# Performance work log

Hardware: AMD Instinct MI355X
Metric: run time of the kernel (lower is better)

The kernel has to match this reference:

```python
import jax, jax.numpy as jnp
import numpy as np

N_NODES = 4096
N_EDGES = 131072
IN_DIM = 40
HID = 128
OUT = 128
GAT_H = 2
GAT_C = 64
D_MODEL = 128
N_HEAD = 4
FF_DIM = 2048
N_LAYERS = 2
EPS = 1e-5
NEG_SLOPE = 0.2


def _layer_norm(x, g, b):
    mu = x.mean(-1, keepdims=True)
    var = ((x - mu) ** 2).mean(-1, keepdims=True)
    return (x - mu) / jnp.sqrt(var + EPS) * g + b


def _gat_conv(h, src, dst, W, a_src, a_dst, bias):
    # PyG GATConv, concat=True, eval mode (no dropout). Self loops already in (src, dst).
    N = h.shape[0]
    xw = (h @ W.T).reshape(N, GAT_H, GAT_C)          # [N, H, C]
    al_src = (xw * a_src).sum(-1)                     # [N, H]
    al_dst = (xw * a_dst).sum(-1)                     # [N, H]
    e = jax.nn.leaky_relu(al_src[src] + al_dst[dst], NEG_SLOPE)  # [E, H]
    # segment softmax over incoming edges of each dst node
    m = jax.ops.segment_max(e, dst, num_segments=N)
    ex = jnp.exp(e - m[dst])
    s = jax.ops.segment_sum(ex, dst, num_segments=N)
    alpha = ex / (s[dst] + 1e-16)                     # [E, H]
    out = jax.ops.segment_sum(xw[src] * alpha[..., None], dst, num_segments=N)
    return out.reshape(N, GAT_H * GAT_C) + bias


def _encoder_layer(x, p):
    # post-norm nn.TransformerEncoderLayer, relu FFN, eval mode
    (in_w, in_b, out_w, out_b, ln1_g, ln1_b,
     ff_w1, ff_b1, ff_w2, ff_b2, ln2_g, ln2_b) = p
    S, E = x.shape
    Dh = E // N_HEAD
    qkv = x @ in_w.T + in_b                           # [S, 3E]
    q, k, v = [t.reshape(S, N_HEAD, Dh) for t in jnp.split(qkv, 3, axis=-1)]
    scores = jnp.einsum('shd,thd->hst', q, k) / jnp.asarray(np.sqrt(Dh), x.dtype)
    attn = jax.nn.softmax(scores, axis=-1)            # [H, S, S]
    o = jnp.einsum('hst,thd->shd', attn, v).reshape(S, E) @ out_w.T + out_b
    x = _layer_norm(x + o, ln1_g, ln1_b)
    ff = jax.nn.relu(x @ ff_w1.T + ff_b1) @ ff_w2.T + ff_b2
    return _layer_norm(x + ff, ln2_g, ln2_b)


def _forward(floats, edge_index):
    (x, enc_w1, enc_b1, enc_w2, enc_b2,
     gat_w, gat_asrc, gat_adst, gat_b,
     l0_in_w, l0_in_b, l0_out_w, l0_out_b, l0_ln1_g, l0_ln1_b,
     l0_ff_w1, l0_ff_b1, l0_ff_w2, l0_ff_b2, l0_ln2_g, l0_ln2_b,
     l1_in_w, l1_in_b, l1_out_w, l1_out_b, l1_ln1_g, l1_ln1_b,
     l1_ff_w1, l1_ff_b1, l1_ff_w2, l1_ff_b2, l1_ln2_g, l1_ln2_b) = floats
    N = x.shape[0]
    # encoder MLP
    h = jax.nn.relu(x @ enc_w1.T + enc_b1) @ enc_w2.T + enc_b2
    # add one self loop per node (GATConv add_self_loops semantics)
    loop = jnp.arange(N, dtype=edge_index.dtype)
    src = jnp.concatenate([edge_index[0], loop])
    dst = jnp.concatenate([edge_index[1], loop])
    h = _gat_conv(h, src, dst, gat_w, gat_asrc, gat_adst, gat_b)
    layers = [
        (l0_in_w, l0_in_b, l0_out_w, l0_out_b, l0_ln1_g, l0_ln1_b,
         l0_ff_w1, l0_ff_b1, l0_ff_w2, l0_ff_b2, l0_ln2_g, l0_ln2_b),
        (l1_in_w, l1_in_b, l1_out_w, l1_out_b, l1_ln1_g, l1_ln1_b,
         l1_ff_w1, l1_ff_b1, l1_ff_w2, l1_ff_b2, l1_ln2_g, l1_ln2_b),
    ]
    for p in layers:
        h = _encoder_layer(h, p)
    return h


def setup_inputs() -> dict:
    key = jax.random.key(0)
    ks = jax.random.split(key, 40)
    s = 0.05
    inp = {}
    inp['x'] = jax.random.normal(ks[0], (N_NODES, IN_DIM), dtype=jnp.float32)
    # edges with src != dst (self loops added inside reference)
    src = jax.random.randint(ks[1], (N_EDGES,), 0, N_NODES)
    off = jax.random.randint(ks[2], (N_EDGES,), 1, N_NODES)
    dst = (src + off) % N_NODES
    inp['edge_index'] = jnp.stack([src, dst]).astype(jnp.int64)
    inp['enc_w1'] = jax.random.normal(ks[3], (HID, IN_DIM)) * s
    inp['enc_b1'] = jnp.zeros((HID,), jnp.float32)
    inp['enc_w2'] = jax.random.normal(ks[4], (OUT, HID)) * s
    inp['enc_b2'] = jnp.zeros((OUT,), jnp.float32)
    inp['gat_w'] = jax.random.normal(ks[5], (GAT_H * GAT_C, OUT)) * s
    inp['gat_asrc'] = jax.random.normal(ks[6], (GAT_H, GAT_C)) * s
    inp['gat_adst'] = jax.random.normal(ks[7], (GAT_H, GAT_C)) * s
    inp['gat_b'] = jnp.zeros((GAT_H * GAT_C,), jnp.float32)
    for i in range(N_LAYERS):
        k = jax.random.split(ks[8 + i], 8)
        inp[f'l{i}_in_w'] = jax.random.normal(k[0], (3 * D_MODEL, D_MODEL)) * s
        inp[f'l{i}_in_b'] = jnp.zeros((3 * D_MODEL,), jnp.float32)
        inp[f'l{i}_out_w'] = jax.random.normal(k[1], (D_MODEL, D_MODEL)) * s
        inp[f'l{i}_out_b'] = jnp.zeros((D_MODEL,), jnp.float32)
        inp[f'l{i}_ln1_g'] = jnp.ones((D_MODEL,), jnp.float32)
        inp[f'l{i}_ln1_b'] = jnp.zeros((D_MODEL,), jnp.float32)
        inp[f'l{i}_ff_w1'] = jax.random.normal(k[2], (FF_DIM, D_MODEL)) * s
        inp[f'l{i}_ff_b1'] = jnp.zeros((FF_DIM,), jnp.float32)
        inp[f'l{i}_ff_w2'] = jax.random.normal(k[3], (D_MODEL, FF_DIM)) * s
        inp[f'l{i}_ff_b2'] = jnp.zeros((D_MODEL,), jnp.float32)
        inp[f'l{i}_ln2_g'] = jnp.ones((D_MODEL,), jnp.float32)
        inp[f'l{i}_ln2_b'] = jnp.zeros((D_MODEL,), jnp.float32)
    return inp


def reference(x, edge_index, enc_w1, enc_b1, enc_w2, enc_b2,
              gat_w, gat_asrc, gat_adst, gat_b,
              l0_in_w, l0_in_b, l0_out_w, l0_out_b, l0_ln1_g, l0_ln1_b,
              l0_ff_w1, l0_ff_b1, l0_ff_w2, l0_ff_b2, l0_ln2_g, l0_ln2_b,
              l1_in_w, l1_in_b, l1_out_w, l1_out_b, l1_ln1_g, l1_ln1_b,
              l1_ff_w1, l1_ff_b1, l1_ff_w2, l1_ff_b2, l1_ln2_g, l1_ln2_b):
    floats = (x, enc_w1, enc_b1, enc_w2, enc_b2,
              gat_w, gat_asrc, gat_adst, gat_b,
              l0_in_w, l0_in_b, l0_out_w, l0_out_b, l0_ln1_g, l0_ln1_b,
              l0_ff_w1, l0_ff_b1, l0_ff_w2, l0_ff_b2, l0_ln2_g, l0_ln2_b,
              l1_in_w, l1_in_b, l1_out_w, l1_out_b, l1_ln1_g, l1_ln1_b,
              l1_ff_w1, l1_ff_b1, l1_ff_w2, l1_ff_b2, l1_ln2_g, l1_ln2_b)
    return _forward(floats, edge_index)
```

## Files before the change

### kernel.cpp

```cpp
#include <hip/hip_runtime.h>
#include <hip/hip_bf16.h>

typedef __hip_bfloat16 bf16;

#define N_NODES 4096
#define IN_DIM  40
#define DM      128
#define FF_DIM  2048
#define GAT_H   2
#define GAT_C   64
#define NHEAD   4
#define DH      32
#define LN_EPS  1e-5f
#define KSPLIT  8
#define FSPLIT  4

typedef short s8v __attribute__((ext_vector_type(8)));
typedef float f4v __attribute__((ext_vector_type(4)));

__device__ __forceinline__ float anyload(const void* p, size_t i, int isbf) {
    if (isbf) return __bfloat162float(((const bf16*)p)[i]);
    return ((const float*)p)[i];
}
__device__ __forceinline__ int geti(const int* ei, int i, int is64) {
    return is64 ? ei[2 * (size_t)i] : ei[i];
}
__device__ __forceinline__ ushort tob(float v) {
    bf16 b = __float2bfloat16(v);
    return *(ushort*)&b;
}

__global__ void probe_kernel(const void* ones_vec, const int* ei, int* flags,
                             int* __restrict__ deg) {
    int i = blockIdx.x * 256 + threadIdx.x;
    if (i < N_NODES) deg[i] = 0;
    if (i == 0) {
        unsigned u = ((const unsigned*)ones_vec)[0];
        flags[0] = (u == 0x3F803F80u) ? 1 : 0;
        const unsigned* e = (const unsigned*)ei;
        flags[1] = (e[1] == 0u && e[3] == 0u && e[5] == 0u && e[7] == 0u) ? 1 : 0;
    }
}

__global__ __launch_bounds__(256) void enc1_mfma_kernel(const void* __restrict__ X,
                                                        const void* __restrict__ W,
                                                        const void* __restrict__ bias,
                                                        ushort* __restrict__ Cb,
                                                        const int* __restrict__ flags) {
    const int isbf = flags[0];
    const int t = threadIdx.x;
    const int w = t >> 6, lane = t & 63;
    const int col = lane & 15, quad = lane >> 4;
    const int wr = (w & 1) * 16, wc = (w >> 1) * 32;
    const int row0 = blockIdx.y * 32, col0 = blockIdx.x * 64;
    __shared__ __align__(16) ushort As[32 * 72];
    __shared__ __align__(16) ushort Ws[64 * 72];
    {
        int r = t >> 3, c0 = (t & 7) * 8;
#pragma unroll
        for (int j = 0; j < 8; ++j) {
            int c = c0 + j;
            float v = (c < IN_DIM) ? anyload(X, (size_t)(row0 + r) * IN_DIM + c, isbf) : 0.f;
            As[r * 72 + c] = tob(v);
        }
    }
#pragma unroll
    for (int i = 0; i < 2; ++i) {
        int idx = t + i * 256;
        int r = idx >> 3, c0 = (idx & 7) * 8;
#pragma unroll
        for (int j = 0; j < 8; ++j) {
            int c = c0 + j;
            float v = (c < IN_DIM) ? anyload(W, (size_t)(col0 + r) * IN_DIM + c, isbf) : 0.f;
            Ws[r * 72 + c] = tob(v);
        }
    }
    __syncthreads();
    f4v zero = {0.f, 0.f, 0.f, 0.f};
    f4v acc[2] = {zero, zero};
    s8v a0  = *(const s8v*)&As[(wr + col) * 72 + quad * 8];
    s8v a1  = *(const s8v*)&As[(wr + col) * 72 + 32 + quad * 8];
    s8v b00 = *(const s8v*)&Ws[(wc + col) * 72 + quad * 8];
    s8v b10 = *(const s8v*)&Ws[(wc + 16 + col) * 72 + quad * 8];
    s8v b01 = *(const s8v*)&Ws[(wc + col) * 72 + 32 + quad * 8];
    s8v b11 = *(const s8v*)&Ws[(wc + 16 + col) * 72 + 32 + quad * 8];
    acc[0] = __builtin_amdgcn_mfma_f32_16x16x32_bf16(a0, b00, acc[0], 0, 0, 0);
    acc[1] = __builtin_amdgcn_mfma_f32_16x16x32_bf16(a0, b10, acc[1], 0, 0, 0);
    acc[0] = __builtin_amdgcn_mfma_f32_16x16x32_bf16(a1, b01, acc[0], 0, 0, 0);
    acc[1] = __builtin_amdgcn_mfma_f32_16x16x32_bf16(a1, b11, acc[1], 0, 0, 0);
#pragma unroll
    for (int nc = 0; nc < 2; ++nc) {
        int cc = col0 + wc + nc * 16 + col;
        float bv = anyload(bias, cc, isbf);
#pragma unroll
        for (int r = 0; r < 4; ++r) {
            int rr = row0 + wr + quad * 4 + r;
            float v = fmaxf(acc[nc][r] + bv, 0.f);
            Cb[(size_t)rr * DM + cc] = tob(v);
        }
    }
}

#define K128STR 136
__global__ __launch_bounds__(256) void k128_gemm_kernel(const ushort* __restrict__ A,
                                                        const void* __restrict__ W,
                                                        const void* __restrict__ bias,
                                                        ushort* __restrict__ Cb,
                                                        ushort* __restrict__ vtb,
                                                        int N,
                                                        const int* __restrict__ flags,
                                                        int relu) {
    const int isbf = flags[0];
    const int t = threadIdx.x;
    const int w = t >> 6, lane = t & 63;
    const int col = lane & 15, quad = lane >> 4;
    const int wc = w * 16;
    const int row0 = blockIdx.y * 16, col0 = blockIdx.x * 64;
    __shared__ __align__(16) ushort As[16 * K128STR];
    __shared__ __align__(16) ushort Ws[64 * K128STR];
    {
        int ar = t >> 4, ac = (t & 15) * 8;
        *(uint4*)&As[ar * K128STR + ac] = *(const uint4*)&A[(size_t)(row0 + ar) * DM + ac];
    }
    if (isbf) {
        const ushort* Wb = (const ushort*)W;
#pragma unroll
        for (int i = 0; i < 4; ++i) {
            int idx = t + i * 256;
            int r = idx >> 4, c = (idx & 15) * 8;
            *(uint4*)&Ws[r * K128STR + c] = *(const uint4*)&Wb[(size_t)(col0 + r) * DM + c];
        }
    } else {
        const float* Wf = (const float*)W;
#pragma unroll
        for (int i = 0; i < 4; ++i) {
            int idx = t + i * 256;
            int r = idx >> 4, c = (idx & 15) * 8;
#pragma unroll
            for (int j = 0; j < 8; ++j)
                Ws[r * K128STR + c + j] = tob(Wf[(size_t)(col0 + r) * DM + c + j]);
        }
    }
    __syncthreads();
    f4v acc = {0.f, 0.f, 0.f, 0.f};
#pragma unroll
    for (int j = 0; j < 4; ++j) {
        s8v a = *(const s8v*)&As[col * K128STR + j * 32 + quad * 8];
        s8v b = *(const s8v*)&Ws[(wc + col) * K128STR + j * 32 + quad * 8];
        acc = __builtin_amdgcn_mfma_f32_16x16x32_bf16(a, b, acc, 0, 0, 0);
    }
    int cc = col0 + wc + col;
    float bv = bias ? anyload(bias, cc, isbf) : 0.f;
#pragma unroll
    for (int r = 0; r < 4; ++r) {
        int rr = row0 + quad * 4 + r;
        float v = acc[r] + bv;
        if (relu) v = fmaxf(v, 0.f);
        Cb[(size_t)rr * N + cc] = tob(v);
        if (vtb && cc >= 256) vtb[(size_t)(cc - 256) * N_NODES + rr] = tob(v);
    }
}

__global__ __launch_bounds__(256) void enc2_gat_kernel(const ushort* __restrict__ hid,
                                                       const void* __restrict__ w2,
                                                       const void* __restrict__ b2,
                                                       const void* __restrict__ gw,
                                                       const void* __restrict__ asrc,
                                                       const void* __restrict__ adst,
                                                       ushort* __restrict__ hb,
                                                       float* __restrict__ xw,
                                                       float* __restrict__ als,
                                                       float* __restrict__ ald,
                                                       const int* __restrict__ flags) {
    const int isbf = flags[0];
    const int t = threadIdx.x;
    const int w = t >> 6, lane = t & 63;
    const int col = lane & 15, quad = lane >> 4;
    const int row0 = blockIdx.x * 16;
    __shared__ __align__(16) ushort As[16 * K128STR];
    __shared__ __align__(16) ushort Ws[128 * K128STR];
    __shared__ float Cs[16][132];

    {
        int ar = t >> 4, ac = (t & 15) * 8;
        *(uint4*)&As[ar * K128STR + ac] = *(const uint4*)&hid[(size_t)(row0 + ar) * DM + ac];
    }
    if (isbf) {
        const ushort* Wb = (const ushort*)w2;
#pragma unroll
        for (int i = 0; i < 8; ++i) {
            int idx = t + i * 256;
            int r = idx >> 4, c = (idx & 15) * 8;
            *(uint4*)&Ws[r * K128STR + c] = *(const uint4*)&Wb[(size_t)r * DM + c];
        }
    } else {
        const float* Wf = (const float*)w2;
#pragma unroll
        for (int i = 0; i < 8; ++i) {
            int idx = t + i * 256;
            int r = idx >> 4, c = (idx & 15) * 8;
#pragma unroll
            for (int j = 0; j < 8; ++j)
                Ws[r * K128STR + c + j] = tob(Wf[(size_t)r * DM + c + j]);
        }
    }
    __syncthreads();
    f4v zero = {0.f, 0.f, 0.f, 0.f};
    f4v acc[2] = {zero, zero};
#pragma unroll
    for (int nc = 0; nc < 2; ++nc)
#pragma unroll
        for (int j = 0; j < 4; ++j) {
            s8v a = *(const s8v*)&As[col * K128STR + j * 32 + quad * 8];
            s8v b = *(const s8v*)&Ws[(w * 32 + nc * 16 + col) * K128STR + j * 32 + quad * 8];
            acc[nc] = __builtin_amdgcn_mfma_f32_16x16x32_bf16(a, b, acc[nc], 0, 0, 0);
        }
    __syncthreads();
#pragma unroll
    for (int nc = 0; nc < 2; ++nc) {
        int cc = w * 32 + nc * 16 + col;
        float bv = anyload(b2, cc, isbf);
#pragma unroll
        for (int r = 0; r < 4; ++r) {
            int row = quad * 4 + r;
            float v = acc[nc][r] + bv;
            ushort hv = tob(v);
            hb[(size_t)(row0 + row) * DM + cc] = hv;
            As[row * K128STR + cc] = hv;
        }
    }
    if (isbf) {
        const ushort* Wb = (const ushort*)gw;
#pragma unroll
        for (int i = 0; i < 8; ++i) {
            int idx = t + i * 256;
            int r = idx >> 4, c = (idx & 15) * 8;
            *(uint4*)&Ws[r * K128STR + c] = *(const uint4*)&Wb[(size_t)r * DM + c];
        }
    } else {
        const float* Wf = (const float*)gw;
#pragma unroll
        for (int i = 0; i < 8; ++i) {
            int idx = t + i * 256;
            int r = idx >> 4, c = (idx & 15) * 8;
#pragma unroll
            for (int j = 0; j < 8; ++j)
                Ws[r * K128STR + c + j] = tob(Wf[(size_t)r * DM + c + j]);
        }
    }
    __syncthreads();
    f4v acc2[2] = {zero, zero};
#pragma unroll
    for (int nc = 0; nc < 2; ++nc)
#pragma unroll
        for (int j = 0; j < 4; ++j) {
            s8v a = *(const s8v*)&As[col * K128STR + j * 32 + quad * 8];
            s8v b = *(const s8v*)&Ws[(w * 32 + nc * 16 + col) * K128STR + j * 32 + quad * 8];
            acc2[nc] = __builtin_amdgcn_mfma_f32_16x16x32_bf16(a, b, acc2[nc], 0, 0, 0);
        }
#pragma unroll
    for (int nc = 0; nc < 2; ++nc) {
        int cc = w * 32 + nc * 16 + col;
#pragma unroll
        for (int r = 0; r < 4; ++r) {
            int row = quad * 4 + r;
            float v = acc2[nc][r];
            xw[(size_t)(row0 + row) * DM + cc] = v;
            Cs[row][cc] = v;
        }
    }
    __syncthreads();
#pragma unroll
    for (int rr = 0; rr < 4; ++rr) {
        int row = w * 4 + rr;
        float x0 = Cs[row][lane], x1 = Cs[row][64 + lane];
        float s0 = x0 * anyload(asrc, lane, isbf);
        float d0 = x0 * anyload(adst, lane, isbf);
        float s1 = x1 * anyload(asrc, 64 + lane, isbf);
        float d1 = x1 * anyload(adst, 64 + lane, isbf);
#pragma unroll
        for (int o = 32; o >= 1; o >>= 1) {
            s0 += __shfl_xor(s0, o); d0 += __shfl_xor(d0, o);
            s1 += __shfl_xor(s1, o); d1 += __shfl_xor(d1, o);
        }
        if (lane == 0) {
            int n = row0 + row;
            als[n * 2 + 0] = s0; ald[n * 2 + 0] = d0;
            als[n * 2 + 1] = s1; ald[n * 2 + 1] = d1;
        }
    }
}

__global__ __launch_bounds__(256) void oproj_ln_kernel(const float* __restrict__ pO,
                                                       const float* __restrict__ pL,
                                                       const void* __restrict__ W,
                                                       const void* __restrict__ bias,
                                                       float* __restrict__ h,
                                                       ushort* __restrict__ hb,
                                                       const void* __restrict__ g,
                                                       const void* __restrict__ b,
                                                       const int* __restrict__ flags) {
    const int isbf = flags[0];
    const int t = threadIdx.x;
    const int w = t >> 6, lane = t & 63;
    const int col = lane & 15, quad = lane >> 4;
    const int row0 = blockIdx.x * 16;
    __shared__ __align__(16) ushort As[16 * K128STR];
    __shared__ __align__(16) ushort Ws[128 * K128STR];
    __shared__ float Cs[16][132];

    {
        int ar = t >> 4, ac = (t & 15) * 8;
        int rr = row0 + ar;
        int hh = ac >> 5, d0 = ac & 31;
        size_t qi0 = ((size_t)rr) * NHEAD + hh;
        float lsum = 0.f;
        float osum[8] = {};
#pragma unroll
        for (int kz = 0; kz < KSPLIT; ++kz) {
            size_t qi = qi0 + (size_t)kz * N_NODES * NHEAD;
            lsum += pL[qi];
            const float* po = &pO[qi * 32 + d0];
#pragma unroll
            for (int j = 0; j < 8; ++j) osum[j] += po[j];
        }
        float inv = 1.f / lsum;
#pragma unroll
        for (int j = 0; j < 8; ++j) As[ar * K128STR + ac + j] = tob(osum[j] * inv);
    }
    if (isbf) {
        const ushort* Wb = (const ushort*)W;
#pragma unroll
        for (int i = 0; i < 8; ++i) {
            int idx = t + i * 256;
            int r = idx >> 4, c = (idx & 15) * 8;
            *(uint4*)&Ws[r * K128STR + c] = *(const uint4*)&Wb[(size_t)r * DM + c];
        }
    } else {
        const float* Wf = (const float*)W;
#pragma unroll
        for (int i = 0; i < 8; ++i) {
            int idx = t + i * 256;
            int r = idx >> 4, c = (idx & 15) * 8;
#pragma unroll
            for (int j = 0; j < 8; ++j)
                Ws[r * K128STR + c + j] = tob(Wf[(size_t)r * DM + c + j]);
        }
    }
    __syncthreads();
    f4v zero = {0.f, 0.f, 0.f, 0.f};
    f4v acc[2] = {zero, zero};
#pragma unroll
    for (int nc = 0; nc < 2; ++nc)
#pragma unroll
        for (int j = 0; j < 4; ++j) {
            s8v a = *(const s8v*)&As[col * K128STR + j * 32 + quad * 8];
            s8v b = *(const s8v*)&Ws[(w * 32 + nc * 16 + col) * K128STR + j * 32 + quad * 8];
            acc[nc] = __builtin_amdgcn_mfma_f32_16x16x32_bf16(a, b, acc[nc], 0, 0, 0);
        }
#pragma unroll
    for (int nc = 0; nc < 2; ++nc) {
        int cc = w * 32 + nc * 16 + col;
        float bv = bias ? anyload(bias, cc, isbf) : 0.f;
#pragma unroll
        for (int r = 0; r < 4; ++r)
            Cs[quad * 4 + r][cc] = acc[nc][r] + bv;
    }
    __syncthreads();
#pragma unroll
    for (int rr = 0; rr < 4; ++rr) {
        int row = w * 4 + rr;
        size_t base = (size_t)(row0 + row) * DM;
        float v0 = h[base + lane] + Cs[row][lane];
        float v1 = h[base + 64 + lane] + Cs[row][64 + lane];
        float s = v0 + v1;
#pragma unroll
        for (int o = 32; o >= 1; o >>= 1) s += __shfl_xor(s, o);
        float mu = s * (1.f / DM);
        float d0 = v0 - mu, d1 = v1 - mu;
        float q = d0 * d0 + d1 * d1;
#pragma unroll
        for (int o = 32; o >= 1; o >>= 1) q += __shfl_xor(q, o);
        float rstd = rsqrtf(q * (1.f / DM) + LN_EPS);
        float o0 = d0 * rstd * anyload(g, lane, isbf) + anyload(b, lane, isbf);
        float o1 = d1 * rstd * anyload(g, 64 + lane, isbf) + anyload(b, 64 + lane, isbf);
        h[base + lane] = o0;       h[base + 64 + lane] = o1;
        hb[base + lane] = tob(o0); hb[base + 64 + lane] = tob(o1);
    }
}

__global__ __launch_bounds__(256) void mfma_gemm_splitk_kernel(const ushort* __restrict__ A,
                                                               const void* __restrict__ W,
                                                               float* __restrict__ Cpart,
                                                               int M, int N, int K, int kchunk,
                                                               const int* __restrict__ flags) {
    const int isbf = flags[0];
    const int t = threadIdx.x;
    const int w = t >> 6, lane = t & 63;
    const int col = lane & 15, quad = lane >> 4;
    const int wr = (w & 1) * 16, wc = (w >> 1) * 32;
    const int row0 = blockIdx.y * 32, col0 = blockIdx.x * 64;
    const int kz = blockIdx.z;
    const int k_beg = kz * kchunk, k_end = k_beg + kchunk;
    __shared__ __align__(16) ushort As[32 * 72];
    __shared__ __align__(16) ushort Ws[64 * 72];
    f4v zero = {0.f, 0.f, 0.f, 0.f};
    f4v acc[2] = {zero, zero};
    const int ar = t >> 3, ac = (t & 7) * 8;
    for (int k0 = k_beg; k0 < k_end; k0 += 64) {
        __syncthreads();
        *(uint4*)&As[ar * 72 + ac] = *(const uint4*)&A[(size_t)(row0 + ar) * K + k0 + ac];
        if (isbf) {
            const ushort* Wb = (const ushort*)W;
#pragma unroll
            for (int i = 0; i < 2; ++i) {
                int idx = t + i * 256;
                int r = idx >> 3, c = (idx & 7) * 8;
                *(uint4*)&Ws[r * 72 + c] = *(const uint4*)&Wb[(size_t)(col0 + r) * K + k0 + c];
            }
        } else {
            const float* Wf = (const float*)W;
#pragma unroll
            for (int i = 0; i < 2; ++i) {
                int idx = t + i * 256;
                int r = idx >> 3, c = (idx & 7) * 8;
#pragma unroll
                for (int j = 0; j < 8; ++j)
                    Ws[r * 72 + c + j] = tob(Wf[(size_t)(col0 + r) * K + k0 + c + j]);
            }
        }
        __syncthreads();
        s8v a0  = *(const s8v*)&As[(wr + col) * 72 + quad * 8];
        s8v a1  = *(const s8v*)&As[(wr + col) * 72 + 32 + quad * 8];
        s8v b00 = *(const s8v*)&Ws[(wc + col) * 72 + quad * 8];
        s8v b10 = *(const s8v*)&Ws[(wc + 16 + col) * 72 + quad * 8];
        s8v b01 = *(const s8v*)&Ws[(wc + col) * 72 + 32 + quad * 8];
        s8v b11 = *(const s8v*)&Ws[(wc + 16 + col) * 72 + 32 + quad * 8];
        acc[0] = __builtin_amdgcn_mfma_f32_16x16x32_bf16(a0, b00, acc[0], 0, 0, 0);
        acc[1] = __builtin_amdgcn_mfma_f32_16x16x32_bf16(a0, b10, acc[1], 0, 0, 0);
        acc[0] = __builtin_amdgcn_mfma_f32_16x16x32_bf16(a1, b01, acc[0], 0, 0, 0);
        acc[1] = __builtin_amdgcn_mfma_f32_16x16x32_bf16(a1, b11, acc[1], 0, 0, 0);
    }
#pragma unroll
    for (int nc = 0; nc < 2; ++nc) {
        int cc = col0 + wc + nc * 16 + col;
#pragma unroll
        for (int r = 0; r < 4; ++r) {
            int rr = row0 + wr + quad * 4 + r;
            Cpart[((size_t)kz * M + rr) * N + cc] = acc[nc][r];
        }
    }
}

__global__ void deg_hist_kernel(const int* __restrict__ ei, int E0,
                                int* __restrict__ deg, const int* __restrict__ flags) {
    const int is64 = flags[1];
    int e = blockIdx.x * 256 + threadIdx.x;
    int E = E0 + N_NODES;
    if (e >= E) return;
    int d = (e < E0) ? geti(ei, E0 + e, is64) : (e - E0);
    atomicAdd(&deg[d], 1);
}

__global__ __launch_bounds__(256) void scan_kernel(const int* __restrict__ deg,
                                                   int* __restrict__ rowptr,
                                                   int* __restrict__ cursor) {
    __shared__ int part[256];
    const int t = threadIdx.x;
    const int base = t * 16;
    int loc[16];
    int s = 0;
#pragma unroll
    for (int i = 0; i < 16; ++i) { loc[i] = s; s += deg[base + i]; }
    part[t] = s;
    __syncthreads();
    for (int d = 1; d < 256; d <<= 1) {
        int v = (t >= d) ? part[t - d] : 0;
        __syncthreads();
        part[t] += v;
        __syncthreads();
    }
    int prev = (t == 0) ? 0 : part[t - 1];
#pragma unroll
    for (int i = 0; i < 16; ++i) {
        int r = prev + loc[i];
        rowptr[base + i] = r;
        cursor[base + i] = r;
    }
    if (t == 255) rowptr[N_NODES] = part[255];
}

__global__ void scatter_kernel(const int* __restrict__ ei, int E0,
                               int* __restrict__ cursor, int* __restrict__ csr_src,
                               const int* __restrict__ flags) {
    const int is64 = flags[1];
    int e = blockIdx.x * 256 + threadIdx.x;
    int E = E0 + N_NODES;
    if (e >= E) return;
    int s = (e < E0) ? geti(ei, e, is64) : (e - E0);
    int d = (e < E0) ? geti(ei, E0 + e, is64) : (e - E0);
    int pos = atomicAdd(&cursor[d], 1);
    csr_src[pos] = s;
}

__global__ __launch_bounds__(256) void gat_gather_kernel(const int* __restrict__ rowptr,
                                                         const int* __restrict__ csr_src,
                                                         const float* __restrict__ als,
                                                         const float* __restrict__ ald,
                                                         const float* __restrict__ xw,
                                                         const void* __restrict__ gat_b,
                                                         float* __restrict__ hg,
                                                         ushort* __restrict__ hgb,
                                                         const int* __restrict__ flags) {
    const int isbf = flags[0];
    const int idx = blockIdx.x * 4 + (threadIdx.x >> 6);
    const int lane = threadIdx.x & 63;
    const int d = idx >> 1, hh = idx & 1;
    const int beg = rowptr[d], end = rowptr[d + 1];
    const float aldv = ald[d * 2 + hh];

    float mx = -3.0e38f;
    for (int i = beg + lane; i < end; i += 64) {
        int s = csr_src[i];
        float v = als[s * 2 + hh] + aldv;
        v = (v > 0.f) ? v : 0.2f * v;
        mx = fmaxf(mx, v);
    }
#pragma unroll
    for (int o = 32; o >= 1; o >>= 1) mx = fmaxf(mx, __shfl_xor(mx, o));
    float sm = 0.f;
    for (int i = beg + lane; i < end; i += 64) {
        int s = csr_src[i];
        float v = als[s * 2 + hh] + aldv;
        v = (v > 0.f) ? v : 0.2f * v;
        sm += __expf(v - mx);
    }
#pragma unroll
    for (int o = 32; o >= 1; o >>= 1) sm += __shfl_xor(sm, o);
    const float inv = 1.f / (sm + 1e-16f);

    float o_acc = 0.f;
    for (int i = beg; i < end; ++i) {
        int s = csr_src[i];
        float v = als[s * 2 + hh] + aldv;
        v = (v > 0.f) ? v : 0.2f * v;
        float alpha = __expf(v - mx) * inv;
        o_acc += alpha * xw[(size_t)s * DM + hh * GAT_C + lane];
    }
    float outv = o_acc + anyload(gat_b, hh * GAT_C + lane, isbf);
    size_t off = (size_t)d * DM + hh * GAT_C + lane;
    hg[off] = outv;
    hgb[off] = tob(outv);
}

#define KSTR 40
#define VSTR 136
#define PSTR 136
__global__ __launch_bounds__(256) void attn_mfma_kernel(const ushort* __restrict__ qkvb,
                                                        const ushort* __restrict__ vtb,
                                                        float* __restrict__ pO,
                                                        float* __restrict__ pL) {
    const int hh = blockIdx.y;
    const int kz = blockIdx.z;
    const int t = threadIdx.x;
    const int w = t >> 6;
    const int lane = t & 63;
    const int col = lane & 15;
    const int quad = lane >> 4;
    const int qr = blockIdx.x * 64 + w * 16;

    __shared__ __align__(16) ushort Ks[128 * KSTR];
    __shared__ __align__(16) ushort Vt[32 * VSTR];
    __shared__ __align__(16) ushort Pl[4][16 * PSTR];

    s8v aq = *(const s8v*)&qkvb[(size_t)(qr + col) * 384 + hh * 32 + quad * 8];

    f4v zero = {0.f, 0.f, 0.f, 0.f};
    f4v of[2] = {zero, zero};
    float lacc[4] = {0.f, 0.f, 0.f, 0.f};
    const float scale = 0.17677669529663687f;
    const int k_beg = kz * (N_NODES / KSPLIT);
    const int k_end = k_beg + (N_NODES / KSPLIT);

    for (int kt = k_beg; kt < k_end; kt += 128) {
        __syncthreads();
        for (int idx = t; idx < 512; idx += 256) {
            int r = idx >> 2, c = (idx & 3) * 8;
            *(uint4*)&Ks[r * KSTR + c] =
                *(const uint4*)&qkvb[(size_t)(kt + r) * 384 + 128 + hh * 32 + c];
        }
        for (int idx = t; idx < 512; idx += 256) {
            int d = idx >> 4, c = (idx & 15) * 8;
            *(uint4*)&Vt[d * VSTR + c] =
                *(const uint4*)&vtb[(size_t)(hh * 32 + d) * N_NODES + kt + c];
        }
        __syncthreads();

        f4v sf[8];
#pragma unroll
        for (int kb = 0; kb < 8; ++kb) {
            s8v bk = *(const s8v*)&Ks[(kb * 16 + col) * KSTR + quad * 8];
            sf[kb] = __builtin_amdgcn_mfma_f32_16x16x32_bf16(aq, bk, zero, 0, 0, 0);
        }
#pragma unroll
        for (int kb = 0; kb < 8; ++kb) {
#pragma unroll
            for (int r = 0; r < 4; ++r) {
                float p = __expf(sf[kb][r] * scale);
                lacc[r] += p;
                Pl[w][(quad * 4 + r) * PSTR + kb * 16 + col] = tob(p);
            }
        }
#pragma unroll
        for (int kc = 0; kc < 4; ++kc) {
            s8v ap = *(const s8v*)&Pl[w][col * PSTR + kc * 32 + quad * 8];
#pragma unroll
            for (int nc = 0; nc < 2; ++nc) {
                s8v bv = *(const s8v*)&Vt[(nc * 16 + col) * VSTR + kc * 32 + quad * 8];
                of[nc] = __builtin_amdgcn_mfma_f32_16x16x32_bf16(ap, bv, of[nc], 0, 0, 0);
            }
        }
    }
#pragma unroll
    for (int r = 0; r < 4; ++r) {
        float lv = lacc[r];
#pragma unroll
        for (int off = 1; off <= 8; off <<= 1) lv += __shfl_xor(lv, off);
        int row = quad * 4 + r;
        size_t qi = ((size_t)kz * N_NODES + qr + row) * NHEAD + hh;
#pragma unroll
        for (int nc = 0; nc < 2; ++nc)
            pO[qi * 32 + nc * 16 + col] = of[nc][r];
        if (col == 0) pL[qi] = lv;
    }
}

__global__ __launch_bounds__(256) void ln4_kernel(float* __restrict__ h,
                                                  const float* __restrict__ pC,
                                                  const void* __restrict__ fbias,
                                                  ushort* __restrict__ hb,
                                                  const void* __restrict__ g, const void* __restrict__ b,
                                                  void* __restrict__ outp,
                                                  const int* __restrict__ flags) {
    const int isbf = flags[0];
    const int row = blockIdx.x * 4 + (threadIdx.x >> 6);
    const int lane = threadIdx.x & 63;
    const size_t base = (size_t)row * DM;
    float y0 = anyload(fbias, lane, isbf), y1 = anyload(fbias, 64 + lane, isbf);
#pragma unroll
    for (int kz = 0; kz < FSPLIT; ++kz) {
        size_t pb = (size_t)kz * N_NODES * DM + base;
        y0 += pC[pb + lane];
        y1 += pC[pb + 64 + lane];
    }
    float v0 = h[base + lane] + y0;
    float v1 = h[base + 64 + lane] + y1;
    float s = v0 + v1;
#pragma unroll
    for (int o = 32; o >= 1; o >>= 1) s += __shfl_xor(s, o);
    float mu = s * (1.f / DM);
    float d0 = v0 - mu, d1 = v1 - mu;
    float q = d0 * d0 + d1 * d1;
#pragma unroll
    for (int o = 32; o >= 1; o >>= 1) q += __shfl_xor(q, o);
    float rstd = rsqrtf(q * (1.f / DM) + LN_EPS);
    float o0 = d0 * rstd * anyload(g, lane, isbf) + anyload(b, lane, isbf);
    float o1 = d1 * rstd * anyload(g, 64 + lane, isbf) + anyload(b, 64 + lane, isbf);
    h[base + lane] = o0;       h[base + 64 + lane] = o1;
    hb[base + lane] = tob(o0); hb[base + 64 + lane] = tob(o1);
    if (outp) {
        if (isbf) {
            ((ushort*)outp)[base + lane] = tob(o0);
            ((ushort*)outp)[base + 64 + lane] = tob(o1);
        } else {
            ((float*)outp)[base + lane] = o0;
            ((float*)outp)[base + 64 + lane] = o1;
        }
    }
}

extern "C" void kernel_launch(void* const* d_in, const int* in_sizes, int n_in,
                              void* d_out, int out_size, void* d_ws, size_t ws_size,
                              hipStream_t stream) {
    const void* x        = d_in[0];
    const int*  ei       = (const int*)d_in[1];
    const void* enc_w1   = d_in[2];
    const void* enc_b1   = d_in[3];
    const void* enc_w2   = d_in[4];
    const void* enc_b2   = d_in[5];
    const void* gat_w    = d_in[6];
    const void* gat_asrc = d_in[7];
    const void* gat_adst = d_in[8];
    const void* gat_b    = d_in[9];
    const void *in_w[2], *in_b[2], *out_w[2], *out_b[2], *ln1_g[2], *ln1_b[2];
    const void *ff_w1[2], *ff_b1[2], *ff_w2[2], *ff_b2[2], *ln2_g[2], *ln2_b[2];
    for (int L = 0; L < 2; ++L) {
        int base = 10 + L * 12;
        in_w[L]  = d_in[base + 0];
        in_b[L]  = d_in[base + 1];
        out_w[L] = d_in[base + 2];
        out_b[L] = d_in[base + 3];
        ln1_g[L] = d_in[base + 4];
        ln1_b[L] = d_in[base + 5];
        ff_w1[L] = d_in[base + 6];
        ff_b1[L] = d_in[base + 7];
        ff_w2[L] = d_in[base + 8];
        ff_b2[L] = d_in[base + 9];
        ln2_g[L] = d_in[base + 10];
        ln2_b[L] = d_in[base + 11];
    }
    const int E0 = in_sizes[1] / 2;
    const int E  = E0 + N_NODES;
    const size_t NN = N_NODES;

    int*    flags   = (int*)d_ws;
    float*  h       = (float*)d_ws + 64;
    ushort* hb      = (ushort*)(h + NN * DM);
    ushort* hid     = hb + NN * DM;
    ushort* qkvb    = hid + NN * DM;
    ushort* vtb     = qkvb + NN * 384;
    float*  pO      = (float*)(vtb + NN * DM);
    float*  pL      = pO + (size_t)KSPLIT * NN * NHEAD * 32;
    float*  pC      = pL + (size_t)KSPLIT * NN * NHEAD;
    ushort* ff1b    = (ushort*)(pC + (size_t)FSPLIT * NN * DM);
    float*  xw      = (float*)(ff1b + NN * FF_DIM);
    float*  als     = xw + NN * DM;
    float*  ald     = als + NN * GAT_H;
    int*    deg     = (int*)(ald + NN * GAT_H);
    int*    rowptr  = deg + N_NODES;
    int*    cursor  = rowptr + N_NODES + 1;
    int*    csr_src = cursor + N_NODES;

    dim3 blk(256);

    probe_kernel<<<dim3(16), blk, 0, stream>>>(ln1_g[0], ei, flags, deg);
    deg_hist_kernel<<<dim3((E + 255) / 256), blk, 0, stream>>>(ei, E0, deg, flags);
    scan_kernel<<<dim3(1), blk, 0, stream>>>(deg, rowptr, cursor);
    scatter_kernel<<<dim3((E + 255) / 256), blk, 0, stream>>>(ei, E0, cursor, csr_src, flags);

    enc1_mfma_kernel<<<dim3(DM / 64, N_NODES / 32), blk, 0, stream>>>(
        x, enc_w1, enc_b1, hid, flags);
    enc2_gat_kernel<<<dim3(N_NODES / 16), blk, 0, stream>>>(
        hid, enc_w2, enc_b2, gat_w, gat_asrc, gat_adst, hb, xw, als, ald, flags);
    gat_gather_kernel<<<dim3(N_NODES * GAT_H / 4), blk, 0, stream>>>(
        rowptr, csr_src, als, ald, xw, gat_b, h, hb, flags);

    for (int L = 0; L < 2; ++L) {
        k128_gemm_kernel<<<dim3(3 * DM / 64, N_NODES / 16), blk, 0, stream>>>(
            hb, in_w[L], in_b[L], qkvb, vtb, 3 * DM, flags, 0);
        attn_mfma_kernel<<<dim3(N_NODES / 64, NHEAD, KSPLIT), blk, 0, stream>>>(
            qkvb, vtb, pO, pL);
        oproj_ln_kernel<<<dim3(N_NODES / 16), blk, 0, stream>>>(
            pO, pL, out_w[L], out_b[L], h, hb, ln1_g[L], ln1_b[L], flags);
        k128_gemm_kernel<<<dim3(FF_DIM / 64, N_NODES / 16), blk, 0, stream>>>(
            hb, ff_w1[L], ff_b1[L], ff1b, nullptr, FF_DIM, flags, 1);
        mfma_gemm_splitk_kernel<<<dim3(DM / 64, N_NODES / 32, FSPLIT), blk, 0, stream>>>(
            ff1b, ff_w2[L], pC, N_NODES, DM, FF_DIM, FF_DIM / FSPLIT, flags);
        ln4_kernel<<<dim3(N_NODES / 4), blk, 0, stream>>>(
            h, pC, ff_b2[L], hb, ln2_g[L], ln2_b[L],
            (L == 1) ? d_out : nullptr, flags);
    }
}
```

Baseline: 341.5 us.

## Fuse FFN up-projection, ReLU, down-projection and LayerNorm into one kernel

After: 401.4 us. 1.18x slower.

```diff
diff --git a/kernel.cpp b/kernel.cpp
--- a/kernel.cpp
+++ b/kernel.cpp
@@ -13,7 +13,6 @@
 #define DH      32
 #define LN_EPS  1e-5f
 #define KSPLIT  8
-#define FSPLIT  4
 
 typedef short s8v __attribute__((ext_vector_type(8)));
 typedef float f4v __attribute__((ext_vector_type(4)));
@@ -389,65 +388,137 @@
     }
 }
 
-__global__ __launch_bounds__(256) void mfma_gemm_splitk_kernel(const ushort* __restrict__ A,
-                                                               const void* __restrict__ W,
-                                                               float* __restrict__ Cpart,
-                                                               int M, int N, int K, int kchunk,
-                                                               const int* __restrict__ flags) {
+#define FSTR 136
+__global__ __launch_bounds__(256) void ffn_ln_kernel(const ushort* __restrict__ hb_in,
+                                                     const void* __restrict__ w1,
+                                                     const void* __restrict__ b1,
+                                                     const void* __restrict__ w2,
+                                                     const void* __restrict__ b2,
+                                                     float* __restrict__ h,
+                                                     ushort* __restrict__ hb,
+                                                     const void* __restrict__ g,
+                                                     const void* __restrict__ b,
+                                                     void* __restrict__ outp,
+                                                     const int* __restrict__ flags) {
     const int isbf = flags[0];
     const int t = threadIdx.x;
     const int w = t >> 6, lane = t & 63;
     const int col = lane & 15, quad = lane >> 4;
-    const int wr = (w & 1) * 16, wc = (w >> 1) * 32;
-    const int row0 = blockIdx.y * 32, col0 = blockIdx.x * 64;
-    const int kz = blockIdx.z;
-    const int k_beg = kz * kchunk, k_end = k_beg + kchunk;
-    __shared__ __align__(16) ushort As[32 * 72];
-    __shared__ __align__(16) ushort Ws[64 * 72];
+    const int row0 = blockIdx.x * 16;
+    __shared__ __align__(16) ushort As[16 * FSTR];
+    __shared__ __align__(16) ushort W1s[64 * FSTR];
+    __shared__ __align__(16) ushort W2s[128 * 72];
+    __shared__ __align__(16) ushort Pl[16 * 72];
+    __shared__ float Cs[16][132];
+
+    {
+        int ar = t >> 4, ac = (t & 15) * 8;
+        *(uint4*)&As[ar * FSTR + ac] = *(const uint4*)&hb_in[(size_t)(row0 + ar) * DM + ac];
+    }
     f4v zero = {0.f, 0.f, 0.f, 0.f};
     f4v acc[2] = {zero, zero};
-    const int ar = t >> 3, ac = (t & 7) * 8;
-    for (int k0 = k_beg; k0 < k_end; k0 += 64) {
+
+    for (int kc = 0; kc < FF_DIM / 64; ++kc) {
         __syncthreads();
-        *(uint4*)&As[ar * 72 + ac] = *(const uint4*)&A[(size_t)(row0 + ar) * K + k0 + ac];
         if (isbf) {
-            const ushort* Wb = (const ushort*)W;
-#pragma unroll
-            for (int i = 0; i < 2; ++i) {
+            const ushort* Wb = (const ushort*)w1 + (size_t)kc * 64 * DM;
+#pragma unroll
+            for (int i = 0; i < 4; ++i) {
+                int idx = t + i * 256;
+                int r = idx >> 4, c = (idx & 15) * 8;
+                *(uint4*)&W1s[r * FSTR + c] = *(const uint4*)&Wb[(size_t)r * DM + c];
+            }
+        } else {
+            const float* Wf = (const float*)w1 + (size_t)kc * 64 * DM;
+#pragma unroll
+            for (int i = 0; i < 4; ++i) {
+                int idx = t + i * 256;
+                int r = idx >> 4, c = (idx & 15) * 8;
+#pragma unroll
+                for (int j = 0; j < 8; ++j)
+                    W1s[r * FSTR + c + j] = tob(Wf[(size_t)r * DM + c + j]);
+            }
+        }
+        if (isbf) {
+            const ushort* Wb = (const ushort*)w2 + (size_t)kc * 64;
+#pragma unroll
+            for (int i = 0; i < 4; ++i) {
                 int idx = t + i * 256;
                 int r = idx >> 3, c = (idx & 7) * 8;
-                *(uint4*)&Ws[r * 72 + c] = *(const uint4*)&Wb[(size_t)(col0 + r) * K + k0 + c];
+                *(uint4*)&W2s[r * 72 + c] = *(const uint4*)&Wb[(size_t)r * FF_DIM + c];
             }
         } else {
-            const float* Wf = (const float*)W;
-#pragma unroll
-            for (int i = 0; i < 2; ++i) {
+            const float* Wf = (const float*)w2 + (size_t)kc * 64;
+#pragma unroll
+            for (int i = 0; i < 4; ++i) {
                 int idx = t + i * 256;
                 int r = idx >> 3, c = (idx & 7) * 8;
 #pragma unroll
                 for (int j = 0; j < 8; ++j)
-                    Ws[r * 72 + c + j] = tob(Wf[(size_t)(col0 + r) * K + k0 + c + j]);
+                    W2s[r * 72 + c + j] = tob(Wf[(size_t)r * FF_DIM + c + j]);
             }
         }
         __syncthreads();
-        s8v a0  = *(const s8v*)&As[(wr + col) * 72 + quad * 8];
-        s8v a1  = *(const s8v*)&As[(wr + col) * 72 + 32 + quad * 8];
-        s8v b00 = *(const s8v*)&Ws[(wc + col) * 72 + quad * 8];
-        s8v b10 = *(const s8v*)&Ws[(wc + 16 + col) * 72 + quad * 8];
-        s8v b01 = *(const s8v*)&Ws[(wc + col) * 72 + 32 + quad * 8];
-        s8v b11 = *(const s8v*)&Ws[(wc + 16 + col) * 72 + 32 + quad * 8];
-        acc[0] = __builtin_amdgcn_mfma_f32_16x16x32_bf16(a0, b00, acc[0], 0, 0, 0);
-        acc[1] = __builtin_amdgcn_mfma_f32_16x16x32_bf16(a0, b10, acc[1], 0, 0, 0);
-        acc[0] = __builtin_amdgcn_mfma_f32_16x16x32_bf16(a1, b01, acc[0], 0, 0, 0);
-        acc[1] = __builtin_amdgcn_mfma_f32_16x16x32_bf16(a1, b11, acc[1], 0, 0, 0);
+        f4v pacc = zero;
+#pragma unroll
+        for (int j = 0; j < 4; ++j) {
+            s8v a  = *(const s8v*)&As[col * FSTR + j * 32 + quad * 8];
+            s8v bw = *(const s8v*)&W1s[(w * 16 + col) * FSTR + j * 32 + quad * 8];
+            pacc = __builtin_amdgcn_mfma_f32_16x16x32_bf16(a, bw, pacc, 0, 0, 0);
+        }
+        float b1v = anyload(b1, kc * 64 + w * 16 + col, isbf);
+#pragma unroll
+        for (int r = 0; r < 4; ++r) {
+            float p = fmaxf(pacc[r] + b1v, 0.f);
+            Pl[(quad * 4 + r) * 72 + w * 16 + col] = tob(p);
+        }
+        __syncthreads();
+        s8v a0 = *(const s8v*)&Pl[col * 72 + quad * 8];
+        s8v a1 = *(const s8v*)&Pl[col * 72 + 32 + quad * 8];
+#pragma unroll
+        for (int nc = 0; nc < 2; ++nc) {
+            s8v b0 = *(const s8v*)&W2s[(w * 32 + nc * 16 + col) * 72 + quad * 8];
+            s8v b1r = *(const s8v*)&W2s[(w * 32 + nc * 16 + col) * 72 + 32 + quad * 8];
+            acc[nc] = __builtin_amdgcn_mfma_f32_16x16x32_bf16(a0, b0, acc[nc], 0, 0, 0);
+            acc[nc] = __builtin_amdgcn_mfma_f32_16x16x32_bf16(a1, b1r, acc[nc], 0, 0, 0);
+        }
     }
 #pragma unroll
     for (int nc = 0; nc < 2; ++nc) {
-        int cc = col0 + wc + nc * 16 + col;
-#pragma unroll
-        for (int r = 0; r < 4; ++r) {
-            int rr = row0 + wr + quad * 4 + r;
-            Cpart[((size_t)kz * M + rr) * N + cc] = acc[nc][r];
+        int cc = w * 32 + nc * 16 + col;
+        float bv = anyload(b2, cc, isbf);
+#pragma unroll
+        for (int r = 0; r < 4; ++r)
+            Cs[quad * 4 + r][cc] = acc[nc][r] + bv;
+    }
+    __syncthreads();
+#pragma unroll
+    for (int rr = 0; rr < 4; ++rr) {
+        int row = w * 4 + rr;
+        size_t base = (size_t)(row0 + row) * DM;
+        float v0 = h[base + lane] + Cs[row][lane];
+        float v1 = h[base + 64 + lane] + Cs[row][64 + lane];
+        float s = v0 + v1;
+#pragma unroll
+        for (int o = 32; o >= 1; o >>= 1) s += __shfl_xor(s, o);
+        float mu = s * (1.f / DM);
+        float d0 = v0 - mu, d1 = v1 - mu;
+        float q = d0 * d0 + d1 * d1;
+#pragma unroll
+        for (int o = 32; o >= 1; o >>= 1) q += __shfl_xor(q, o);
+        float rstd = rsqrtf(q * (1.f / DM) + LN_EPS);
+        float o0 = d0 * rstd * anyload(g, lane, isbf) + anyload(b, lane, isbf);
+        float o1 = d1 * rstd * anyload(g, 64 + lane, isbf) + anyload(b, 64 + lane, isbf);
+        h[base + lane] = o0;       h[base + 64 + lane] = o1;
+        hb[base + lane] = tob(o0); hb[base + 64 + lane] = tob(o1);
+        if (outp) {
+            if (isbf) {
+                ((ushort*)outp)[base + lane] = tob(o0);
+                ((ushort*)outp)[base + 64 + lane] = tob(o1);
+            } else {
+                ((float*)outp)[base + lane] = o0;
+                ((float*)outp)[base + 64 + lane] = o1;
+            }
         }
     }
 }
@@ -632,50 +703,6 @@
         for (int nc = 0; nc < 2; ++nc)
             pO[qi * 32 + nc * 16 + col] = of[nc][r];
         if (col == 0) pL[qi] = lv;
-    }
-}
-
-__global__ __launch_bounds__(256) void ln4_kernel(float* __restrict__ h,
-                                                  const float* __restrict__ pC,
-                                                  const void* __restrict__ fbias,
-                                                  ushort* __restrict__ hb,
-                                                  const void* __restrict__ g, const void* __restrict__ b,
-                                                  void* __restrict__ outp,
-                                                  const int* __restrict__ flags) {
-    const int isbf = flags[0];
-    const int row = blockIdx.x * 4 + (threadIdx.x >> 6);
-    const int lane = threadIdx.x & 63;
-    const size_t base = (size_t)row * DM;
-    float y0 = anyload(fbias, lane, isbf), y1 = anyload(fbias, 64 + lane, isbf);
-#pragma unroll
-    for (int kz = 0; kz < FSPLIT; ++kz) {
-        size_t pb = (size_t)kz * N_NODES * DM + base;
-        y0 += pC[pb + lane];
-        y1 += pC[pb + 64 + lane];
-    }
-    float v0 = h[base + lane] + y0;
-    float v1 = h[base + 64 + lane] + y1;
-    float s = v0 + v1;
-#pragma unroll
-    for (int o = 32; o >= 1; o >>= 1) s += __shfl_xor(s, o);
-    float mu = s * (1.f / DM);
-    float d0 = v0 - mu, d1 = v1 - mu;
-    float q = d0 * d0 + d1 * d1;
-#pragma unroll
-    for (int o = 32; o >= 1; o >>= 1) q += __shfl_xor(q, o);
-    float rstd = rsqrtf(q * (1.f / DM) + LN_EPS);
-    float o0 = d0 * rstd * anyload(g, lane, isbf) + anyload(b, lane, isbf);
-    float o1 = d1 * rstd * anyload(g, 64 + lane, isbf) + anyload(b, 64 + lane, isbf);
-    h[base + lane] = o0;       h[base + 64 + lane] = o1;
-    hb[base + lane] = tob(o0); hb[base + 64 + lane] = tob(o1);
-    if (outp) {
-        if (isbf) {
-            ((ushort*)outp)[base + lane] = tob(o0);
-            ((ushort*)outp)[base + 64 + lane] = tob(o1);
-        } else {
-            ((float*)outp)[base + lane] = o0;
-            ((float*)outp)[base + 64 + lane] = o1;
-        }
     }
 }
 
@@ -721,9 +748,7 @@
     ushort* vtb     = qkvb + NN * 384;
     float*  pO      = (float*)(vtb + NN * DM);
     float*  pL      = pO + (size_t)KSPLIT * NN * NHEAD * 32;
-    float*  pC      = pL + (size_t)KSPLIT * NN * NHEAD;
-    ushort* ff1b    = (ushort*)(pC + (size_t)FSPLIT * NN * DM);
-    float*  xw      = (float*)(ff1b + NN * FF_DIM);
+    float*  xw      = pL + (size_t)KSPLIT * NN * NHEAD;
     float*  als     = xw + NN * DM;
     float*  ald     = als + NN * GAT_H;
     int*    deg     = (int*)(ald + NN * GAT_H);
@@ -752,12 +777,8 @@
             qkvb, vtb, pO, pL);
         oproj_ln_kernel<<<dim3(N_NODES / 16), blk, 0, stream>>>(
             pO, pL, out_w[L], out_b[L], h, hb, ln1_g[L], ln1_b[L], flags);
-        k128_gemm_kernel<<<dim3(FF_DIM / 64, N_NODES / 16), blk, 0, stream>>>(
-            hb, ff_w1[L], ff_b1[L], ff1b, nullptr, FF_DIM, flags, 1);
-        mfma_gemm_splitk_kernel<<<dim3(DM / 64, N_NODES / 32, FSPLIT), blk, 0, stream>>>(
-            ff1b, ff_w2[L], pC, N_NODES, DM, FF_DIM, FF_DIM / FSPLIT, flags);
-        ln4_kernel<<<dim3(N_NODES / 4), blk, 0, stream>>>(
-            h, pC, ff_b2[L], hb, ln2_g[L], ln2_b[L],
+        ffn_ln_kernel<<<dim3(N_NODES / 16), blk, 0, stream>>>(
+            hb, ff_w1[L], ff_b1[L], ff_w2[L], ff_b2[L], h, hb, ln2_g[L], ln2_b[L],
             (L == 1) ? d_out : nullptr, flags);
     }
 }
```
